# Kernel tuning notes

Measured on AMD Instinct MI355X. Metric: run time of the kernel, lower is better.

Reference implementation:

```python
import jax, jax.numpy as jnp
import numpy as np

N = 100000
E = 600000
H = 128
G = 64          # number of graphs
LN_EPS = 1e-5


def setup_inputs() -> dict:
    key = jax.random.key(0)
    ks = jax.random.split(key, 16)
    node = jax.random.normal(ks[0], (N, H), dtype=jnp.float32)
    edge_index = jax.random.randint(ks[1], (2, E), 0, N, dtype=jnp.int64)
    edge_attr = jax.random.normal(ks[2], (E, 1), dtype=jnp.float32)
    batch_ptr = jnp.sort(jax.random.randint(ks[3], (N,), 0, G, dtype=jnp.int64))
    s = 1.0 / np.sqrt(H)
    params = dict(
        eps=jnp.float32(0.0),  # GINConv train_eps=True, init 0
        W1=jax.random.uniform(ks[4], (H, H), jnp.float32, -s, s),
        b1=jnp.zeros((H,), jnp.float32),
        g1=jnp.ones((H,), jnp.float32), be1=jnp.zeros((H,), jnp.float32),
        W2=jax.random.uniform(ks[5], (H, H), jnp.float32, -s, s),
        b2=jnp.zeros((H,), jnp.float32),
        g2=jnp.ones((H,), jnp.float32), be2=jnp.zeros((H,), jnp.float32),
        W3=jax.random.uniform(ks[6], (H, H), jnp.float32, -s, s),
        b3=jnp.zeros((H,), jnp.float32),
        ln_w=jnp.ones((H,), jnp.float32), ln_b=jnp.zeros((H,), jnp.float32),
    )
    return dict(node=node, edge_index=edge_index, edge_attr=edge_attr,
                batch_ptr=batch_ptr, **params)


def _layernorm(x, g, b):
    mu = x.mean(-1, keepdims=True)
    var = ((x - mu) ** 2).mean(-1, keepdims=True)
    return (x - mu) * jax.lax.rsqrt(var + LN_EPS) * g + b


def _forward(node, edge_index, batch_ptr, eps, W1, b1, g1, be1, W2, b2, g2, be2,
             W3, b3, ln_w, ln_b):
    src, dst = edge_index[0], edge_index[1]
    # GIN sum aggregation: scatter-add neighbor features to targets
    agg = jax.ops.segment_sum(node[src], dst, num_segments=N)  # [N, H]
    h = (1.0 + eps) * node + agg
    # 3-layer MLP (PyG MLP: lin -> LayerNorm -> ReLU, final lin plain)
    h = jax.nn.relu(_layernorm(h @ W1 + b1, g1, be1))
    h = jax.nn.relu(_layernorm(h @ W2 + b2, g2, be2))
    h = h @ W3 + b3
    # PyG graph-mode LayerNorm: normalize over all nodes+features per graph
    cnt = jax.ops.segment_sum(jnp.ones((N,), h.dtype), batch_ptr, num_segments=G)
    norm = jnp.maximum(cnt * H, 1.0)                       # [G]
    mean = jax.ops.segment_sum(h.sum(-1), batch_ptr, num_segments=G) / norm
    hc = h - mean[batch_ptr][:, None]
    var = jax.ops.segment_sum((hc * hc).sum(-1), batch_ptr, num_segments=G) / norm
    out = hc * jax.lax.rsqrt(var + LN_EPS)[batch_ptr][:, None] * ln_w + ln_b
    return jax.nn.relu(out)


def reference(node, edge_index, edge_attr, batch_ptr, eps, W1, b1, g1, be1,
              W2, b2, g2, be2, W3, b3, ln_w, ln_b):
    del edge_attr  # accepted by GIN_Layer.forward but unused
    return _forward(node, edge_index, batch_ptr, eps, W1, b1, g1, be1,
                    W2, b2, g2, be2, W3, b3, ln_w, ln_b)
```

## Files before the change

kernel.cpp:

```cpp
#include <hip/hip_runtime.h>

#define N_NODES 100000
#define N_EDGES 600000
#define H 128
#define G_NUM 64
#define LN_EPS 1e-5f

#define WSTR 136

#define NTILES ((N_NODES + 63) / 64)

#define SCAN_CHUNK 1024
#define SCAN_NB ((N_NODES + SCAN_CHUNK - 1) / SCAN_CHUNK)
#define HIST_NB ((N_EDGES + 255) / 256)
#define CVT_NB ((N_NODES * H / 8 + 255) / 256)
#define FILL_NB ((N_EDGES + 255) / 256)
#define WT_NB ((3 * 16384 + 255) / 256)

#define SCR_MAX 272

#define WT_IOFF   900612
#define NBF_IOFF  925192
#define H0_BF_IOFF (NBF_IOFF + N_NODES * (H / 2))
#define NEEDED_BF  ((size_t)(H0_BF_IOFF + N_NODES * (H / 2)) * 4)

typedef __attribute__((ext_vector_type(8))) short short8;
typedef __attribute__((ext_vector_type(4))) float floatx4;

__device__ __forceinline__ unsigned short f2bf(float x) {
    unsigned int u = __float_as_uint(x);
    u += 0x7fffu + ((u >> 16) & 1u);
    return (unsigned short)(u >> 16);
}

__global__ __launch_bounds__(256) void hist_cvt_kernel(
    const int* __restrict__ ei, int* __restrict__ deg,
    const float* __restrict__ node, unsigned int* __restrict__ node_bf)
{
    int gb = blockIdx.x;
    if (gb < HIST_NB) {
        int e = gb * 256 + threadIdx.x;
        if (e >= N_EDGES) return;
        atomicAdd(&deg[ei[N_EDGES + e]], 1);
    } else {
        int i = (gb - HIST_NB) * 256 + threadIdx.x;
        if (i >= N_NODES * H / 8) return;
        float4 a = ((const float4*)node)[i * 2];
        float4 b = ((const float4*)node)[i * 2 + 1];
        uint4 p;
        p.x = (unsigned)f2bf(a.x) | ((unsigned)f2bf(a.y) << 16);
        p.y = (unsigned)f2bf(a.z) | ((unsigned)f2bf(a.w) << 16);
        p.z = (unsigned)f2bf(b.x) | ((unsigned)f2bf(b.y) << 16);
        p.w = (unsigned)f2bf(b.z) | ((unsigned)f2bf(b.w) << 16);
        ((uint4*)node_bf)[i] = p;
    }
}

__global__ __launch_bounds__(256) void scan1_kernel(
    const int* __restrict__ deg, int* __restrict__ off,
    int* __restrict__ blksum)
{
    __shared__ int sA[256], sB[256];
    const int tid = threadIdx.x;
    const int base = blockIdx.x * SCAN_CHUNK + tid * 4;
    int v[4];
#pragma unroll
    for (int j = 0; j < 4; ++j) {
        int i = base + j;
        v[j] = (i < N_NODES) ? deg[i] : 0;
    }
    int tsum = v[0] + v[1] + v[2] + v[3];
    int* a = sA; int* b = sB;
    a[tid] = tsum;
    __syncthreads();
#pragma unroll
    for (int o = 1; o < 256; o <<= 1) {
        int t = a[tid] + ((tid >= o) ? a[tid - o] : 0);
        b[tid] = t;
        __syncthreads();
        int* tmp = a; a = b; b = tmp;
    }
    int run = a[tid] - tsum;
#pragma unroll
    for (int j = 0; j < 4; ++j) {
        int i = base + j;
        if (i < N_NODES) off[i] = run;
        run += v[j];
    }
    if (tid == 255) blksum[blockIdx.x] = a[255];
}

__global__ __launch_bounds__(256) void scan23_kernel(
    int* __restrict__ off, const int* __restrict__ blksum,
    int* __restrict__ cursor)
{
    __shared__ int sA[128], sB[128];
    const int tid = threadIdx.x;
    if (tid < 128) sA[tid] = (tid < SCAN_NB) ? blksum[tid] : 0;
    __syncthreads();
    int* a = sA; int* b = sB;
#pragma unroll
    for (int o = 1; o < 128; o <<= 1) {
        int t = 0;
        if (tid < 128) t = a[tid] + ((tid >= o) ? a[tid - o] : 0);
        __syncthreads();
        if (tid < 128) b[tid] = t;
        __syncthreads();
        int* tmp = a; a = b; b = tmp;
    }
    int excl = 0;
    if (tid < 128) excl = a[tid] - ((tid < SCAN_NB) ? blksum[tid] : 0);
    __syncthreads();
    if (tid < 128) sA[tid] = excl;
    __syncthreads();

    int i = blockIdx.x * 256 + tid;
    if (i < N_NODES) {
        int val = off[i] + sA[i >> 10];
        off[i] = val;
        cursor[i] = val;
    }
    if (i == 0) off[N_NODES] = N_EDGES;
}

__global__ __launch_bounds__(256) void fill_wt_kernel(
    const int* __restrict__ ei, int* __restrict__ cursor,
    int* __restrict__ csr,
    const float* __restrict__ W1, const float* __restrict__ W2,
    const float* __restrict__ W3, unsigned short* __restrict__ WT)
{
    int gb = blockIdx.x;
    if (gb < FILL_NB) {
        int e = gb * 256 + threadIdx.x;
        if (e >= N_EDGES) return;
        int dst = ei[N_EDGES + e];
        int pos = atomicAdd(&cursor[dst], 1);
        csr[pos] = ei[e];
    } else {
        int idx = (gb - FILL_NB) * 256 + threadIdx.x;
        if (idx >= 3 * 16384) return;
        int l = idx >> 14, r = idx & 16383;
        int frag = r >> 3, j = r & 7;
        int lane = frag & 63, ktnt = frag >> 6;
        int kt = ktnt & 3, nt = ktnt >> 2;
        int c = lane & 15, q = lane >> 4;
        int n = nt * 16 + c;
        int k = kt * 32 + q * 8 + j;
        const float* W = (l == 0) ? W1 : ((l == 1) ? W2 : W3);
        WT[l * 16384 + r] = f2bf(W[k * 128 + n]);
    }
}

template <bool NBF>
__global__ __launch_bounds__(256) void gather_kernel(
    const float* __restrict__ node, const unsigned int* __restrict__ nbf,
    const int* __restrict__ off, const int* __restrict__ csr,
    const float* __restrict__ epsp, unsigned int* __restrict__ h0)
{
    __shared__ int scr4[4][SCR_MAX];
    const int tid = threadIdx.x;
    const int w = tid >> 6, lane = tid & 63;
    const int n0 = blockIdx.x * 64 + w * 16;
    const float epsv = 1.0f + epsp[0];

    const float2* np2 = (const float2*)node;

    int oidx = n0 + ((lane < 17) ? lane : 16);
    if (oidx > N_NODES) oidx = N_NODES;
    const int offl = off[oidx];
    const int e_begin = __shfl(offl, 0);
    const int e_end   = __shfl(offl, 16);
    const int cnt = e_end - e_begin;

    int* scr = scr4[w];
    const bool use_scr = (cnt <= SCR_MAX);
    if (use_scr) {
        for (int k = lane; k < cnt; k += 64) scr[k] = csr[e_begin + k];
        __threadfence_block();
    }

    for (int i = 0; i < 16; ++i) {
        int n = n0 + i;
        if (n >= N_NODES) break;
        const int kb = __shfl(offl, i) - e_begin;
        const int ke = __shfl(offl, i + 1) - e_begin;

        float a0, a1;
        if constexpr (NBF) {
            unsigned uo = nbf[(size_t)n * 64 + lane];
            a0 = epsv * __uint_as_float(uo << 16);
            a1 = epsv * __uint_as_float(uo & 0xffff0000u);
        } else {
            float2 own = np2[(size_t)n * 64 + lane];
            a0 = epsv * own.x;
            a1 = epsv * own.y;
        }

        for (int k = kb; k < ke; k += 8) {
            const int m = ke - k;
            if constexpr (NBF) {
                unsigned uu[8];
#pragma unroll
                for (int j = 0; j < 8; ++j) {
                    if (j < m) {
                        int nb = __builtin_amdgcn_readfirstlane(
                            use_scr ? scr[k + j] : csr[e_begin + k + j]);
                        uu[j] = nbf[(size_t)nb * 64 + lane];
                    }
                }
#pragma unroll
                for (int j = 0; j < 8; ++j) {
                    if (j < m) {
                        a0 += __uint_as_float(uu[j] << 16);
                        a1 += __uint_as_float(uu[j] & 0xffff0000u);
                    }
                }
            } else {
                float2 vv[8];
#pragma unroll
                for (int j = 0; j < 8; ++j) {
                    if (j < m) {
                        int nb = __builtin_amdgcn_readfirstlane(
                            use_scr ? scr[k + j] : csr[e_begin + k + j]);
                        vv[j] = np2[(size_t)nb * 64 + lane];
                    }
                }
#pragma unroll
                for (int j = 0; j < 8; ++j) {
                    if (j < m) { a0 += vv[j].x; a1 += vv[j].y; }
                }
            }
        }

        unsigned pk = (unsigned)f2bf(a0) | ((unsigned)f2bf(a1) << 16);
        h0[(size_t)n * 64 + lane] = pk;
    }
}

__device__ __forceinline__ void gemm_frags(const unsigned short* hIn,
                                           const unsigned short* __restrict__ WTl,
                                           floatx4 acc[8], int w, int lane)
{
    const int c = lane & 15, q = lane >> 4;
#pragma unroll
    for (int nt = 0; nt < 8; ++nt) acc[nt] = (floatx4){0.f, 0.f, 0.f, 0.f};
#pragma unroll
    for (int kt = 0; kt < 4; ++kt) {
        short8 a = *(const short8*)&hIn[(w * 16 + c) * WSTR + kt * 32 + q * 8];
#pragma unroll
        for (int nt = 0; nt < 8; ++nt) {
            short8 b = *(const short8*)&WTl[(nt * 256 + kt * 64 + lane) * 8];
            acc[nt] = __builtin_amdgcn_mfma_f32_16x16x32_bf16(a, b, acc[nt], 0, 0, 0);
        }
    }
}

__device__ __forceinline__ void gemm_layer_ln(unsigned short* h,
                                              const unsigned short* __restrict__ WTl,
                                              const float* __restrict__ bias,
                                              const float* __restrict__ g,
                                              const float* __restrict__ be,
                                              int w, int lane)
{
    const int c = lane & 15, q = lane >> 4;
    floatx4 acc[8];
    gemm_frags(h, WTl, acc, w, lane);

    float sum[4] = {0.f, 0.f, 0.f, 0.f};
    float sq[4]  = {0.f, 0.f, 0.f, 0.f};
#pragma unroll
    for (int nt = 0; nt < 8; ++nt) {
        float bv = bias[nt * 16 + c];
#pragma unroll
        for (int i = 0; i < 4; ++i) {
            float vv = acc[nt][i] + bv;
            acc[nt][i] = vv;
            sum[i] += vv; sq[i] += vv * vv;
        }
    }
#pragma unroll
    for (int m = 1; m < 16; m <<= 1) {
#pragma unroll
        for (int i = 0; i < 4; ++i) {
            sum[i] += __shfl_xor(sum[i], m);
            sq[i]  += __shfl_xor(sq[i], m);
        }
    }
    float mu[4], rstd[4];
#pragma unroll
    for (int i = 0; i < 4; ++i) {
        mu[i]   = sum[i] * (1.0f / 128.0f);
        rstd[i] = rsqrtf(sq[i] * (1.0f / 128.0f) - mu[i] * mu[i] + LN_EPS);
    }
#pragma unroll
    for (int nt = 0; nt < 8; ++nt) {
        float gw = g[nt * 16 + c];
        float bw = be[nt * 16 + c];
#pragma unroll
        for (int i = 0; i < 4; ++i) {
            float val = fmaxf(0.f, (acc[nt][i] - mu[i]) * rstd[i] * gw + bw);
            h[(w * 16 + q * 4 + i) * WSTR + nt * 16 + c] = f2bf(val);
        }
    }
}

__global__ __launch_bounds__(256, 4) void mlp_kernel(
    const unsigned int* __restrict__ h0,
    const unsigned short* __restrict__ WT,
    const float* __restrict__ b1, const float* __restrict__ g1,
    const float* __restrict__ be1,
    const float* __restrict__ b2, const float* __restrict__ g2,
    const float* __restrict__ be2,
    const float* __restrict__ b3, const int* __restrict__ batch,
    float* __restrict__ out, float* __restrict__ gstat)
{
    __shared__ unsigned short hA[64 * WSTR];
    __shared__ float prm[7 * 128];
    __shared__ float s_gsum[G_NUM], s_gsq[G_NUM], s_gcnt[G_NUM];

    const int tid = threadIdx.x;
    const int w = tid >> 6, lane = tid & 63;
    const int row0 = blockIdx.x * 64;

    if (tid < G_NUM) { s_gsum[tid] = 0.f; s_gsq[tid] = 0.f; s_gcnt[tid] = 0.f; }
    {
        const float* srcs[7] = {b1, g1, be1, b2, g2, be2, b3};
#pragma unroll
        for (int t = 0; t < 4; ++t) {
            int i = tid + t * 256;
            if (i < 7 * 128) prm[i] = srcs[i >> 7][i & 127];
        }
    }

    {
        const int r = tid >> 2;
        const int q4 = tid & 3;
        uint4* d = (uint4*)(((unsigned int*)hA) + r * (WSTR / 2) + q4 * 16);
        const int row = row0 + r;
        if (row < N_NODES) {
            const uint4* s = (const uint4*)&h0[(size_t)row * 64 + q4 * 16];
#pragma unroll
            for (int k = 0; k < 4; ++k) d[k] = s[k];
        } else {
            uint4 z = make_uint4(0, 0, 0, 0);
#pragma unroll
            for (int k = 0; k < 4; ++k) d[k] = z;
        }
    }
    __syncthreads();

    gemm_layer_ln(hA, WT,         &prm[0],   &prm[128], &prm[256], w, lane);
    gemm_layer_ln(hA, WT + 16384, &prm[384], &prm[512], &prm[640], w, lane);

    {
        const int c = lane & 15, q = lane >> 4;
        floatx4 acc3[8];
        gemm_frags(hA, WT + 32768, acc3, w, lane);
        float sum[4] = {0.f, 0.f, 0.f, 0.f};
        float sq[4]  = {0.f, 0.f, 0.f, 0.f};
#pragma unroll
        for (int nt = 0; nt < 8; ++nt) {
            float bv = prm[768 + nt * 16 + c];
#pragma unroll
            for (int i = 0; i < 4; ++i) {
                float vv = acc3[nt][i] + bv;
                size_t nrow = (size_t)row0 + w * 16 + q * 4 + i;
                if (nrow < N_NODES)
                    out[nrow * H + nt * 16 + c] = vv;
                sum[i] += vv; sq[i] += vv * vv;
            }
        }
#pragma unroll
        for (int m = 1; m < 16; m <<= 1) {
#pragma unroll
            for (int i = 0; i < 4; ++i) {
                sum[i] += __shfl_xor(sum[i], m);
                sq[i]  += __shfl_xor(sq[i], m);
            }
        }
        if (c == 0) {
#pragma unroll
            for (int i = 0; i < 4; ++i) {
                size_t nrow = (size_t)row0 + w * 16 + q * 4 + i;
                if (nrow < N_NODES) {
                    int g = batch[nrow];
                    atomicAdd(&s_gsum[g], sum[i]);
                    atomicAdd(&s_gsq[g], sq[i]);
                    atomicAdd(&s_gcnt[g], 1.0f);
                }
            }
        }
    }
    __syncthreads();
    if (tid < G_NUM && s_gcnt[tid] > 0.f) {
        unsafeAtomicAdd(&gstat[tid], s_gsum[tid]);
        unsafeAtomicAdd(&gstat[G_NUM + tid], s_gsq[tid]);
        unsafeAtomicAdd(&gstat[2 * G_NUM + tid], s_gcnt[tid]);
    }
}

__global__ __launch_bounds__(256) void final_ln_kernel(
    float* __restrict__ h3, const int* __restrict__ batch,
    const float* __restrict__ lnw, const float* __restrict__ lnb,
    const float* __restrict__ gstat)
{
    int idx4 = blockIdx.x * 256 + threadIdx.x;
    if (idx4 >= N_NODES * 32) return;
    int node = idx4 >> 5;
    int c4 = (idx4 & 31) * 4;
    int g = batch[node];
    float s   = gstat[g];
    float qq  = gstat[G_NUM + g];
    float cnt = gstat[2 * G_NUM + g];
    float norm = fmaxf(cnt * (float)H, 1.0f);
    float mean = s / norm;
    float var  = qq / norm - mean * mean;
    float inv  = rsqrtf(var + LN_EPS);
    float4 v = ((const float4*)h3)[idx4];
    float4 w = *(const float4*)&lnw[c4];
    float4 b = *(const float4*)&lnb[c4];
    v.x = fmaxf(0.f, (v.x - mean) * inv * w.x + b.x);
    v.y = fmaxf(0.f, (v.y - mean) * inv * w.y + b.y);
    v.z = fmaxf(0.f, (v.z - mean) * inv * w.z + b.z);
    v.w = fmaxf(0.f, (v.w - mean) * inv * w.w + b.w);
    ((float4*)h3)[idx4] = v;
}

extern "C" void kernel_launch(void* const* d_in, const int* in_sizes, int n_in,
                              void* d_out, int out_size, void* d_ws, size_t ws_size,
                              hipStream_t stream)
{
    const float* node  = (const float*)d_in[0];
    const int*   ei    = (const int*)d_in[1];
    const int*   batch = (const int*)d_in[3];
    const float* epsp  = (const float*)d_in[4];
    const float* W1    = (const float*)d_in[5];
    const float* b1    = (const float*)d_in[6];
    const float* g1    = (const float*)d_in[7];
    const float* be1   = (const float*)d_in[8];
    const float* W2    = (const float*)d_in[9];
    const float* b2    = (const float*)d_in[10];
    const float* g2    = (const float*)d_in[11];
    const float* be2   = (const float*)d_in[12];
    const float* W3    = (const float*)d_in[13];
    const float* b3    = (const float*)d_in[14];
    const float* lnw   = (const float*)d_in[15];
    const float* lnb   = (const float*)d_in[16];

    float* out = (float*)d_out;

    int* base = (int*)d_ws;
    float* gstat  = (float*)d_ws;
    int*   deg    = base + 512;
    int*   off    = deg + N_NODES;
    int*   cursor = off + N_NODES + 1;
    int*   csr    = cursor + N_NODES;
    int*   blksum = csr + N_EDGES;
    unsigned short* WT = (unsigned short*)(base + WT_IOFF);

    const bool use_bf = (ws_size >= NEEDED_BF);
    unsigned int* nbf = (unsigned int*)(base + NBF_IOFF);
    unsigned int* h0  = use_bf ? (unsigned int*)(base + H0_BF_IOFF)
                               : (unsigned int*)(base + NBF_IOFF);

    hipMemsetAsync(d_ws, 0, (512 + N_NODES) * sizeof(int), stream);

    hist_cvt_kernel<<<HIST_NB + (use_bf ? CVT_NB : 0), 256, 0, stream>>>(
        ei, deg, node, nbf);
    scan1_kernel<<<SCAN_NB, 256, 0, stream>>>(deg, off, blksum);
    scan23_kernel<<<(N_NODES + 255) / 256, 256, 0, stream>>>(off, blksum, cursor);
    fill_wt_kernel<<<FILL_NB + WT_NB, 256, 0, stream>>>(ei, cursor, csr,
                                                        W1, W2, W3, WT);

    if (use_bf)
        gather_kernel<true><<<NTILES, 256, 0, stream>>>(node, nbf, off, csr,
                                                        epsp, h0);
    else
        gather_kernel<false><<<NTILES, 256, 0, stream>>>(node, nbf, off, csr,
                                                         epsp, h0);

    mlp_kernel<<<NTILES, 256, 0, stream>>>(h0, WT, b1, g1, be1, b2, g2, be2,
                                           b3, batch, out, gstat);

    final_ln_kernel<<<(N_NODES * 32 + 255) / 256, 256, 0, stream>>>(
        out, batch, lnw, lnb, gstat);
}
```

Measured before the change: 304.1 us.

## Fuse neighbor gather into MLP kernel, writing aggregates directly to LDS

Merges the gather kernel into the MLP kernel, so each block sums its 64 rows' neighbor features and writes the bf16 results straight into the shared-memory tile used by the GEMMs. This removes the round trip of the h0 intermediate buffer through global memory and one kernel launch. It also shrinks the workspace requirement for the bf16 path. In exchange, the block's shared memory grows by the index scratch, which may limit occupancy, and the latency-bound gather now runs in the same kernel as the MFMA phase.

```diff
diff --git a/kernel.cpp b/kernel.cpp
--- a/kernel.cpp
+++ b/kernel.cpp
@@ -21,8 +21,7 @@
 
 #define WT_IOFF   900612
 #define NBF_IOFF  925192
-#define H0_BF_IOFF (NBF_IOFF + N_NODES * (H / 2))
-#define NEEDED_BF  ((size_t)(H0_BF_IOFF + N_NODES * (H / 2)) * 4)
+#define NEEDED_BF ((size_t)(NBF_IOFF + N_NODES * (H / 2)) * 4)
 
 typedef __attribute__((ext_vector_type(8))) short short8;
 typedef __attribute__((ext_vector_type(4))) float floatx4;
@@ -151,92 +150,6 @@
     }
 }
 
-template <bool NBF>
-__global__ __launch_bounds__(256) void gather_kernel(
-    const float* __restrict__ node, const unsigned int* __restrict__ nbf,
-    const int* __restrict__ off, const int* __restrict__ csr,
-    const float* __restrict__ epsp, unsigned int* __restrict__ h0)
-{
-    __shared__ int scr4[4][SCR_MAX];
-    const int tid = threadIdx.x;
-    const int w = tid >> 6, lane = tid & 63;
-    const int n0 = blockIdx.x * 64 + w * 16;
-    const float epsv = 1.0f + epsp[0];
-
-    const float2* np2 = (const float2*)node;
-
-    int oidx = n0 + ((lane < 17) ? lane : 16);
-    if (oidx > N_NODES) oidx = N_NODES;
-    const int offl = off[oidx];
-    const int e_begin = __shfl(offl, 0);
-    const int e_end   = __shfl(offl, 16);
-    const int cnt = e_end - e_begin;
-
-    int* scr = scr4[w];
-    const bool use_scr = (cnt <= SCR_MAX);
-    if (use_scr) {
-        for (int k = lane; k < cnt; k += 64) scr[k] = csr[e_begin + k];
-        __threadfence_block();
-    }
-
-    for (int i = 0; i < 16; ++i) {
-        int n = n0 + i;
-        if (n >= N_NODES) break;
-        const int kb = __shfl(offl, i) - e_begin;
-        const int ke = __shfl(offl, i + 1) - e_begin;
-
-        float a0, a1;
-        if constexpr (NBF) {
-            unsigned uo = nbf[(size_t)n * 64 + lane];
-            a0 = epsv * __uint_as_float(uo << 16);
-            a1 = epsv * __uint_as_float(uo & 0xffff0000u);
-        } else {
-            float2 own = np2[(size_t)n * 64 + lane];
-            a0 = epsv * own.x;
-            a1 = epsv * own.y;
-        }
-
-        for (int k = kb; k < ke; k += 8) {
-            const int m = ke - k;
-            if constexpr (NBF) {
-                unsigned uu[8];
-#pragma unroll
-                for (int j = 0; j < 8; ++j) {
-                    if (j < m) {
-                        int nb = __builtin_amdgcn_readfirstlane(
-                            use_scr ? scr[k + j] : csr[e_begin + k + j]);
-                        uu[j] = nbf[(size_t)nb * 64 + lane];
-                    }
-                }
-#pragma unroll
-                for (int j = 0; j < 8; ++j) {
-                    if (j < m) {
-                        a0 += __uint_as_float(uu[j] << 16);
-                        a1 += __uint_as_float(uu[j] & 0xffff0000u);
-                    }
-                }
-            } else {
-                float2 vv[8];
-#pragma unroll
-                for (int j = 0; j < 8; ++j) {
-                    if (j < m) {
-                        int nb = __builtin_amdgcn_readfirstlane(
-                            use_scr ? scr[k + j] : csr[e_begin + k + j]);
-                        vv[j] = np2[(size_t)nb * 64 + lane];
-                    }
-                }
-#pragma unroll
-                for (int j = 0; j < 8; ++j) {
-                    if (j < m) { a0 += vv[j].x; a1 += vv[j].y; }
-                }
-            }
-        }
-
-        unsigned pk = (unsigned)f2bf(a0) | ((unsigned)f2bf(a1) << 16);
-        h0[(size_t)n * 64 + lane] = pk;
-    }
-}
-
 __device__ __forceinline__ void gemm_frags(const unsigned short* hIn,
                                            const unsigned short* __restrict__ WTl,
                                            floatx4 acc[8], int w, int lane)
@@ -304,8 +217,11 @@
     }
 }
 
-__global__ __launch_bounds__(256, 4) void mlp_kernel(
-    const unsigned int* __restrict__ h0,
+template <bool NBF>
+__global__ __launch_bounds__(256, 4) void fused_kernel(
+    const float* __restrict__ node, const unsigned int* __restrict__ nbf,
+    const int* __restrict__ off, const int* __restrict__ csr,
+    const float* __restrict__ epsp,
     const unsigned short* __restrict__ WT,
     const float* __restrict__ b1, const float* __restrict__ g1,
     const float* __restrict__ be1,
@@ -315,6 +231,7 @@
     float* __restrict__ out, float* __restrict__ gstat)
 {
     __shared__ unsigned short hA[64 * WSTR];
+    __shared__ int scr4[4][SCR_MAX];
     __shared__ float prm[7 * 128];
     __shared__ float s_gsum[G_NUM], s_gsq[G_NUM], s_gcnt[G_NUM];
 
@@ -333,18 +250,82 @@
     }
 
     {
-        const int r = tid >> 2;
-        const int q4 = tid & 3;
-        uint4* d = (uint4*)(((unsigned int*)hA) + r * (WSTR / 2) + q4 * 16);
-        const int row = row0 + r;
-        if (row < N_NODES) {
-            const uint4* s = (const uint4*)&h0[(size_t)row * 64 + q4 * 16];
-#pragma unroll
-            for (int k = 0; k < 4; ++k) d[k] = s[k];
-        } else {
-            uint4 z = make_uint4(0, 0, 0, 0);
-#pragma unroll
-            for (int k = 0; k < 4; ++k) d[k] = z;
+        const float2* np2 = (const float2*)node;
+        const float epsv = 1.0f + epsp[0];
+        const int n0 = row0 + w * 16;
+
+        int oidx = n0 + ((lane < 17) ? lane : 16);
+        if (oidx > N_NODES) oidx = N_NODES;
+        const int offl = off[oidx];
+        const int e_begin = __shfl(offl, 0);
+        const int e_end   = __shfl(offl, 16);
+        const int cnt = e_end - e_begin;
+
+        int* scr = scr4[w];
+        const bool use_scr = (cnt <= SCR_MAX);
+        if (use_scr) {
+            for (int k = lane; k < cnt; k += 64) scr[k] = csr[e_begin + k];
+            __threadfence_block();
+        }
+
+        for (int i = 0; i < 16; ++i) {
+            int n = n0 + i;
+            unsigned int* dst = (unsigned int*)&hA[(w * 16 + i) * WSTR];
+            if (n >= N_NODES) {
+                dst[lane] = 0u;
+                continue;
+            }
+            const int kb = __shfl(offl, i) - e_begin;
+            const int ke = __shfl(offl, i + 1) - e_begin;
+
+            float a0, a1;
+            if constexpr (NBF) {
+                unsigned uo = nbf[(size_t)n * 64 + lane];
+                a0 = epsv * __uint_as_float(uo << 16);
+                a1 = epsv * __uint_as_float(uo & 0xffff0000u);
+            } else {
+                float2 own = np2[(size_t)n * 64 + lane];
+                a0 = epsv * own.x;
+                a1 = epsv * own.y;
+            }
+
+            for (int k = kb; k < ke; k += 8) {
+                const int m = ke - k;
+                if constexpr (NBF) {
+                    unsigned uu[8];
+#pragma unroll
+                    for (int j = 0; j < 8; ++j) {
+                        if (j < m) {
+                            int nb = __builtin_amdgcn_readfirstlane(
+                                use_scr ? scr[k + j] : csr[e_begin + k + j]);
+                            uu[j] = nbf[(size_t)nb * 64 + lane];
+                        }
+                    }
+#pragma unroll
+                    for (int j = 0; j < 8; ++j) {
+                        if (j < m) {
+                            a0 += __uint_as_float(uu[j] << 16);
+                            a1 += __uint_as_float(uu[j] & 0xffff0000u);
+                        }
+                    }
+                } else {
+                    float2 vv[8];
+#pragma unroll
+                    for (int j = 0; j < 8; ++j) {
+                        if (j < m) {
+                            int nb = __builtin_amdgcn_readfirstlane(
+                                use_scr ? scr[k + j] : csr[e_begin + k + j]);
+                            vv[j] = np2[(size_t)nb * 64 + lane];
+                        }
+                    }
+#pragma unroll
+                    for (int j = 0; j < 8; ++j) {
+                        if (j < m) { a0 += vv[j].x; a1 += vv[j].y; }
+                    }
+                }
+            }
+
+            dst[lane] = (unsigned)f2bf(a0) | ((unsigned)f2bf(a1) << 16);
         }
     }
     __syncthreads();
@@ -457,11 +438,9 @@
     int*   csr    = cursor + N_NODES;
     int*   blksum = csr + N_EDGES;
     unsigned short* WT = (unsigned short*)(base + WT_IOFF);
+    unsigned int*  nbf = (unsigned int*)(base + NBF_IOFF);
 
     const bool use_bf = (ws_size >= NEEDED_BF);
-    unsigned int* nbf = (unsigned int*)(base + NBF_IOFF);
-    unsigned int* h0  = use_bf ? (unsigned int*)(base + H0_BF_IOFF)
-                               : (unsigned int*)(base + NBF_IOFF);
 
     hipMemsetAsync(d_ws, 0, (512 + N_NODES) * sizeof(int), stream);
 
@@ -473,14 +452,13 @@
                                                         W1, W2, W3, WT);
 
     if (use_bf)
-        gather_kernel<true><<<NTILES, 256, 0, stream>>>(node, nbf, off, csr,
-                                                        epsp, h0);
+        fused_kernel<true><<<NTILES, 256, 0, stream>>>(
+            node, nbf, off, csr, epsp, WT, b1, g1, be1, b2, g2, be2, b3,
+            batch, out, gstat);
     else
-        gather_kernel<false><<<NTILES, 256, 0, stream>>>(node, nbf, off, csr,
-                                                         epsp, h0);
-
-    mlp_kernel<<<NTILES, 256, 0, stream>>>(h0, WT, b1, g1, be1, b2, g2, be2,
-                                           b3, batch, out, gstat);
+        fused_kernel<false><<<NTILES, 256, 0, stream>>>(
+            node, nbf, off, csr, epsp, WT, b1, g1, be1, b2, g2, be2, b3,
+            batch, out, gstat);
 
     final_ln_kernel<<<(N_NODES * 32 + 255) / 256, 256, 0, stream>>>(
         out, batch, lnw, lnb, gstat);
```

After: 322.6 us. 6.1% more time.
